# Performance work log

Hardware: AMD Instinct MI355X
Metric: run time of the kernel (lower is better)

## Reference

```python
import jax, jax.numpy as jnp
import numpy as np

H = 8          # heads
D_MODEL = 64   # padded embedding dim (power of 2)
D_K = 8        # per-head dim -> NQ=3 qubits
SEQ = 32
NQ = 3
DIM2 = D_K * D_K  # 2*NQ qubit joint space
W_MUL = float(np.sqrt(2.0) * 5 ** (-0.5))  # PQC he_std * lrmul

# ---- static circuit unitaries (qubit 0 = most significant / leftmost in kron) ----

def _cnot(n, c, t):
    dim = 2 ** n
    P = np.zeros((dim, dim), np.complex64)
    for b in range(dim):
        if (b >> (n - 1 - c)) & 1:
            P[b ^ (1 << (n - 1 - t)), b] = 1.0
        else:
            P[b, b] = 1.0
    return P

def _cnot_ring(n):
    U = np.eye(2 ** n, dtype=np.complex64)
    for t in range(n):
        U = _cnot(n, t, (t + 1) % n) @ U  # later gates multiply on the left
    return U

UC6 = jnp.asarray(_cnot_ring(2 * NQ))  # (64,64) entangling ring used by score + sum circuits
MZ6 = jnp.asarray(((-1.0) ** np.array([bin(i).count('1') for i in range(2 ** (2 * NQ))])).astype(np.complex64))  # Z^{otimes 2n} diagonal

# ---- parameterized single-qubit rotations (batched, differentiable) ----

def _rx(t):
    c = jnp.cos(t / 2).astype(jnp.complex64)
    s = jnp.sin(t / 2).astype(jnp.complex64)
    return jnp.stack([jnp.stack([c, -1j * s], -1), jnp.stack([-1j * s, c], -1)], -2)

def _ry(t):
    c = jnp.cos(t / 2).astype(jnp.complex64)
    s = jnp.sin(t / 2).astype(jnp.complex64)
    return jnp.stack([jnp.stack([c, -s], -1), jnp.stack([s, c], -1)], -2)

def _rz(t):
    e = jnp.exp(-0.5j * t.astype(jnp.complex64))
    z = jnp.zeros_like(e)
    return jnp.stack([jnp.stack([e, z], -1), jnp.stack([z, e.conj()], -1)], -2)

def _kron3(a, b, c):
    out = jnp.einsum('...ad,...be,...cf->...abcdef', a, b, c)
    return out.reshape(out.shape[:-6] + (D_K, D_K))

def _pqc_unitaries(w):
    # w: (H, 3, NQ*3); per qubit apply rx, ry, rz -> per-qubit u = Rz@Ry@Rx, circuit = kron
    a = (w * W_MUL).reshape(H, 3, NQ, 3)
    u = _rz(a[..., 2]) @ _ry(a[..., 1]) @ _rx(a[..., 0])  # (H,3,NQ,2,2)
    return _kron3(u[..., 0, :, :], u[..., 1, :, :], u[..., 2, :, :])  # (H,3,dk,dk)

def _forward(x, pqc_w, W1, b1, W2, b2):
    x = jnp.pad(x, ((0, 0), (0, 0), (0, D_MODEL - x.shape[-1])))
    xq = (x @ W1.T + b1)[0]                                    # (S, d_k) linear1
    psi = xq / jnp.sqrt(jnp.sum(xq * xq, -1, keepdims=True))   # amplitude encoding
    rho = (psi[:, :, None] * psi[:, None, :]).astype(jnp.complex64)  # (S,dk,dk) pure-state density matrices
    Upqc = _pqc_unitaries(pqc_w)                               # (H, 3=[q,k,v], dk, dk)
    rqkv = jnp.einsum('hgab,sbc,hgdc->hgsad', Upqc, rho, Upqc.conj())
    qs, ks_, vs = rqkv[:, 0], rqkv[:, 1], rqkv[:, 2]           # (H,S,dk,dk)
    # score_ij = (Re tr(Z^{2n} U (q_i kron k_j) U^dag) + 1)/2 = (Re tr(A (q kron k)) + 1)/2
    A = (UC6.conj().T * MZ6) @ UC6                             # U^dag Z^{2n} U, (64,64)
    A4 = A.reshape(D_K, D_K, D_K, D_K)                         # [(c,d),(a,b)]
    T = jnp.einsum('cdab,hiac->hidb', A4, qs)
    scores = (jnp.einsum('hidb,hjbd->hij', T, ks_).real + 1.0) * 0.5  # (H,S,S)
    # weighted value: per-qubit rx(phi/2) ry(phi/2) rz(phi) with phi=(score-0.5)*2pi
    phi = (scores - 0.5) * (2.0 * jnp.pi)
    u1 = _rz(phi) @ _ry(phi * 0.5) @ _rx(phi * 0.5)            # (H,S,S,2,2)
    Uw = _kron3(u1, u1, u1)                                    # (H,S,S,dk,dk)
    wvs = Uw @ vs[:, None] @ Uw.conj().swapaxes(-1, -2)        # (H,S_i,S_j,dk,dk)

    def step(rho_a, wv_j):
        # cal_sum fold: kron, entangle with CNOT ring, partial-trace out 2nd register
        rho_ab = jnp.einsum('...ij,...kl->...ikjl', rho_a, wv_j).reshape(H, SEQ, DIM2, DIM2)
        out = UC6 @ rho_ab @ UC6.conj().T
        out = out.reshape(H, SEQ, D_K, D_K, D_K, D_K)
        return jnp.einsum('...abcb->...ac', out), None

    rho_fin, _ = jax.lax.scan(step, wvs[:, :, 0], jnp.moveaxis(wvs[:, :, 1:], 2, 0))
    z = jnp.diagonal(rho_fin, axis1=-2, axis2=-1).real         # (H,S,dk) computational-basis probs
    zs = jnp.transpose(z, (1, 0, 2)).reshape(1, SEQ, H * D_K)  # concat heads
    return zs @ W2.T + b2                                      # linear2; dropout = identity (eval)

def setup_inputs():
    key = jax.random.key(0)
    kk = jax.random.split(key, 4)
    x = jax.random.normal(kk[0], (1, SEQ, D_MODEL), jnp.float32)
    pqc_w = jax.random.uniform(kk[1], (H, 3, NQ * 3), jnp.float32, 0.0, 2.0 * float(np.pi))
    W1 = jax.random.normal(kk[2], (D_K, D_MODEL), jnp.float32) / np.sqrt(D_MODEL).astype(np.float32)
    b1 = jnp.zeros((D_K,), jnp.float32)
    W2 = jax.random.normal(kk[3], (D_MODEL, D_MODEL), jnp.float32) / np.sqrt(D_MODEL).astype(np.float32)
    b2 = jnp.zeros((D_MODEL,), jnp.float32)
    return {"x": x, "pqc_w": pqc_w, "W1": W1, "b1": b1, "W2": W2, "b2": b2, "edge_index": 0}

def reference(x, pqc_w, W1, b1, W2, b2, edge_index):
    # edge_index sentinel 0 == None (dense attention path)
    return _forward(x, pqc_w, W1, b1, W2, b2)
```

## Files before the change

kernel.cpp:

```cpp
#include <hip/hip_runtime.h>
#include <hip/hip_bf16.h>

#define NHEAD 8
#define SEQL  32
#define DKQ   8
static constexpr float W_MUL = 0.632455532033675866f;
static constexpr float PI_F  = 3.14159265358979323846f;

#define WS_Q 0
#define WS_K 256
#define WS_V 512
#define WS_Z 4608

__device__ __forceinline__ float2 cmulf(float2 a, float2 b) {
    return make_float2(a.x*b.x - a.y*b.y, a.x*b.y + a.y*b.x);
}
__device__ __forceinline__ float2 caddf(float2 a, float2 b) {
    return make_float2(a.x + b.x, a.y + b.y);
}
__device__ __forceinline__ int sig3(int a) {
    int a2=(a>>2)&1, a1=(a>>1)&1, a0=a&1;
    return (a2<<2) | ((a1^a2)<<1) | (a0^a1);
}

__global__ __launch_bounds__(256) void k1(const float* __restrict__ x,
                                          const float* __restrict__ pqc_w,
                                          const float* __restrict__ W1,
                                          const float* __restrict__ b1,
                                          float* __restrict__ ws) {
    __shared__ float xq[SEQL][DKQ];
    __shared__ float psi[SEQL][DKQ];
    __shared__ float2 U8[64];

    float* Q  = ws + WS_Q;
    float* K  = ws + WS_K;
    float2* V = (float2*)(ws + WS_V);

    const int t = threadIdx.x;
    const int h = blockIdx.x / 3, g = blockIdx.x % 3;

    {
        const int s = t >> 3, k = t & 7;
        const float4* xr = (const float4*)(x  + s*64);
        const float4* wr = (const float4*)(W1 + k*64);
        float acc = b1[k];
        #pragma unroll
        for (int q = 0; q < 16; ++q) {
            float4 xa = xr[q], wa = wr[q];
            acc += xa.x*wa.x + xa.y*wa.y + xa.z*wa.z + xa.w*wa.w;
        }
        xq[s][k] = acc;
    }
    __syncthreads();
    {
        const int s = t >> 3, k = t & 7;
        float ss = 0.f;
        #pragma unroll
        for (int kk = 0; kk < 8; ++kk) ss += xq[s][kk]*xq[s][kk];
        psi[s][k] = xq[s][k] * rsqrtf(ss);
    }

    if (t < 64) {
        float2 u[3][2][2];
        #pragma unroll
        for (int q = 0; q < 3; ++q) {
            int base = h*27 + g*9 + q*3;
            float t0 = pqc_w[base+0] * W_MUL;
            float t1 = pqc_w[base+1] * W_MUL;
            float t2 = pqc_w[base+2] * W_MUL;
            float c0 = cosf(t0*0.5f), s0 = sinf(t0*0.5f);
            float c1 = cosf(t1*0.5f), s1 = sinf(t1*0.5f);
            float cz = cosf(t2*0.5f), sz = sinf(t2*0.5f);
            float2 m00 = make_float2(c1*c0,  s1*s0);
            float2 m01 = make_float2(-s1*c0, -c1*s0);
            float2 m10 = make_float2(s1*c0,  -c1*s0);
            float2 m11 = make_float2(c1*c0,  -s1*s0);
            float2 em = make_float2(cz, -sz), ep = make_float2(cz, sz);
            u[q][0][0] = cmulf(em, m00);  u[q][0][1] = cmulf(em, m01);
            u[q][1][0] = cmulf(ep, m10);  u[q][1][1] = cmulf(ep, m11);
        }
        int r = t >> 3, c = t & 7;
        U8[t] = cmulf(cmulf(u[0][r>>2][c>>2], u[1][(r>>1)&1][(c>>1)&1]),
                      u[2][r&1][c&1]);
    }
    __syncthreads();

    {
        const int lane = t & 63, wv = t >> 6;
        const int sg = lane >> 3, a = lane & 7;
        const int s = wv*8 + sg;
        float2 phi = make_float2(0.f, 0.f);
        #pragma unroll
        for (int b = 0; b < 8; ++b) {
            float pb = psi[s][b];
            float2 ue = U8[a*8 + b];
            phi.x += ue.x * pb;
            phi.y += ue.y * pb;
        }
        if (g == 2) {
            V[(h*SEQL + s)*8 + a] = phi;
        } else {
            float mag = phi.x*phi.x + phi.y*phi.y;
            float sign = (g == 0) ? ((((a>>2) ^ a) & 1) ? -1.f : 1.f)
                                  : (((a>>1) & 1) ? -1.f : 1.f);
            float val = sign * mag;
            val += __shfl_xor(val, 1, 64);
            val += __shfl_xor(val, 2, 64);
            val += __shfl_xor(val, 4, 64);
            if (a == 0) {
                if (g == 0) Q[h*SEQL + s] = val;
                else        K[h*SEQL + s] = val;
            }
        }
    }
}

__global__ __launch_bounds__(64) void k2(const float* __restrict__ ws,
                                         float* __restrict__ Z) {
    __shared__ __align__(16) float2 Carr[SEQL][4][2];
    __shared__ float2 w0s[8];

    const float*  Q  = ws + WS_Q;
    const float*  Kv = ws + WS_K;
    const float2* V  = (const float2*)(ws + WS_V);

    const int l = threadIdx.x;
    const int h = blockIdx.x >> 5, i = blockIdx.x & 31;
    const float qhi = Q[h*SEQL + i];

    {
        const int j = l & 31, half = l >> 5;
        float phi = PI_F * qhi * Kv[h*SEQL + j];
        float c1 = cosf(phi*0.25f), s1 = sinf(phi*0.25f);
        float ch = cosf(phi*0.5f),  sh = sinf(phi*0.5f);
        float2 em = make_float2(ch, -sh), ep = make_float2(ch, sh);
        float sc = s1*c1;
        float2 u00 = cmulf(em, make_float2(c1*c1,  s1*s1));
        float2 u01 = cmulf(em, make_float2(-sc, -sc));
        float2 u10 = cmulf(ep, make_float2(sc, -sc));
        float2 u11 = cmulf(ep, make_float2(c1*c1, -s1*s1));

        float2 w[8];
        #pragma unroll
        for (int b = 0; b < 8; ++b) w[b] = V[(h*SEQL + j)*8 + b];
        #pragma unroll
        for (int p = 0; p < 4; ++p) {
            float2 lo = w[p], hi = w[p+4];
            w[p]   = caddf(cmulf(u00, lo), cmulf(u01, hi));
            w[p+4] = caddf(cmulf(u10, lo), cmulf(u11, hi));
        }
        #pragma unroll
        for (int p = 0; p < 4; ++p) {
            int i0 = ((p >> 1) << 2) | (p & 1);
            float2 lo = w[i0], hi = w[i0+2];
            w[i0]   = caddf(cmulf(u00, lo), cmulf(u01, hi));
            w[i0+2] = caddf(cmulf(u10, lo), cmulf(u11, hi));
        }
        #pragma unroll
        for (int p = 0; p < 4; ++p) {
            float2 lo = w[2*p], hi = w[2*p+1];
            w[2*p]   = caddf(cmulf(u00, lo), cmulf(u01, hi));
            w[2*p+1] = caddf(cmulf(u10, lo), cmulf(u11, hi));
        }

        if (j == 0 && half == 0) {
            #pragma unroll
            for (int b = 0; b < 8; ++b) w0s[b] = w[b];
        }
        const int mset0[4] = {0,3,5,6}, mset1[4] = {1,2,4,7};
        #pragma unroll
        for (int combo = 0; combo < 4; ++combo) {
            int a0 = combo >> 1, c0 = combo & 1;
            float2 acc = make_float2(0.f, 0.f);
            #pragma unroll
            for (int tt = 0; tt < 4; ++tt) {
                int m = half ? mset1[tt] : mset0[tt];
                float2 wx = w[(a0<<2)^m], wy = w[(c0<<2)^m];
                acc.x += wx.x*wy.x + wx.y*wy.y;
                acc.y += wx.y*wy.x - wx.x*wy.y;
            }
            Carr[j][combo][half] = acc;
        }
    }
    __syncthreads();

    const int a = l >> 3, c = l & 7;
    const int combo = ((a & 1) << 1) | (c & 1);
    const int src0 = (sig3(a) << 3) | sig3(c);
    const int src1 = src0 ^ 54;

    float2 wa = w0s[a], wc = w0s[c];
    float rr = wa.x*wc.x + wa.y*wc.y;
    float ri = wa.y*wc.x - wa.x*wc.y;

    for (int j = 1; j < SEQL; ++j) {
        float4 Cv = *((const float4*)&Carr[j][combo][0]);
        float R0r = __shfl(rr, src0, 64);
        float R0i = __shfl(ri, src0, 64);
        float R1r = __shfl(rr, src1, 64);
        float R1i = __shfl(ri, src1, 64);
        float nr = Cv.x*R0r - Cv.y*R0i + Cv.z*R1r - Cv.w*R1i;
        float ni = Cv.x*R0i + Cv.y*R0r + Cv.z*R1i + Cv.w*R1r;
        rr = nr; ri = ni;
    }
    if (a == c) Z[(h*SEQL + i)*8 + a] = rr;
}

__global__ __launch_bounds__(64) void k3(const float* __restrict__ ws,
                                         const float* __restrict__ W2,
                                         const float* __restrict__ b2,
                                         float* __restrict__ out) {
    const float* Z = ws + WS_Z;
    const int s = blockIdx.x, m = threadIdx.x;
    float acc = b2[m];
    #pragma unroll
    for (int cc = 0; cc < 64; ++cc) {
        float z = Z[(cc >> 3)*256 + s*8 + (cc & 7)];
        acc += z * W2[m*64 + cc];
    }
    out[s*64 + m] = acc;
}

extern "C" void kernel_launch(void* const* d_in, const int* in_sizes, int n_in,
                              void* d_out, int out_size, void* d_ws, size_t ws_size,
                              hipStream_t stream) {
    const float* x     = (const float*)d_in[0];
    const float* pqc_w = (const float*)d_in[1];
    const float* W1    = (const float*)d_in[2];
    const float* b1    = (const float*)d_in[3];
    const float* W2    = (const float*)d_in[4];
    const float* b2    = (const float*)d_in[5];

    float* ws = (float*)d_ws;

    hipLaunchKernelGGL(k1, dim3(24),  dim3(256), 0, stream, x, pqc_w, W1, b1, ws);
    hipLaunchKernelGGL(k2, dim3(256), dim3(64),  0, stream, ws, ws + WS_Z);
    hipLaunchKernelGGL(k3, dim3(32),  dim3(64),  0, stream, ws, W2, b2, (float*)d_out);
}
```

Before: 76.86 us.

## Fuse all three stages into one kernel with redundant per-block recompute

Merges the encoding, score/sum circuit and output-projection kernels into a single launch of 32 blocks with 512 threads, one block per query row and one wave per head. Each block recomputes linear1, normalization, the PQC unitaries and the Q/K/V states in shared memory, so no workspace round trips or extra launches are needed. Linear2 is done from shared Z per row with a shuffle reduction. The cost is heavily redundant recomputation in every block and fewer blocks overall.

```diff
diff --git a/kernel.cpp b/kernel.cpp
--- a/kernel.cpp
+++ b/kernel.cpp
@@ -1,16 +1,9 @@
 #include <hip/hip_runtime.h>
-#include <hip/hip_bf16.h>
 
 #define NHEAD 8
 #define SEQL  32
-#define DKQ   8
 static constexpr float W_MUL = 0.632455532033675866f;
 static constexpr float PI_F  = 3.14159265358979323846f;
-
-#define WS_Q 0
-#define WS_K 256
-#define WS_V 512
-#define WS_Z 4608
 
 __device__ __forceinline__ float2 cmulf(float2 a, float2 b) {
     return make_float2(a.x*b.x - a.y*b.y, a.x*b.y + a.y*b.x);
@@ -23,23 +16,27 @@
     return (a2<<2) | ((a1^a2)<<1) | (a0^a1);
 }
 
-__global__ __launch_bounds__(256) void k1(const float* __restrict__ x,
-                                          const float* __restrict__ pqc_w,
-                                          const float* __restrict__ W1,
-                                          const float* __restrict__ b1,
-                                          float* __restrict__ ws) {
-    __shared__ float xq[SEQL][DKQ];
-    __shared__ float psi[SEQL][DKQ];
-    __shared__ float2 U8[64];
-
-    float* Q  = ws + WS_Q;
-    float* K  = ws + WS_K;
-    float2* V = (float2*)(ws + WS_V);
+__global__ __launch_bounds__(512) void kfused(const float* __restrict__ x,
+                                              const float* __restrict__ pqc_w,
+                                              const float* __restrict__ W1,
+                                              const float* __restrict__ b1,
+                                              const float* __restrict__ W2,
+                                              const float* __restrict__ b2,
+                                              float* __restrict__ out) {
+    __shared__ float  xq[SEQL][8];
+    __shared__ float  psi[SEQL][8];
+    __shared__ float2 us[NHEAD][9][4];
+    __shared__ float2 U8s[NHEAD][3][64];
+    __shared__ __align__(16) float2 Carr[NHEAD][SEQL][4][2];
+    __shared__ float2 w0s[NHEAD][8];
+    __shared__ float  Zs[NHEAD][8];
 
     const int t = threadIdx.x;
-    const int h = blockIdx.x / 3, g = blockIdx.x % 3;
-
-    {
+    const int l = t & 63;
+    const int h = t >> 6;
+    const int i = blockIdx.x;
+
+    if (t < 256) {
         const int s = t >> 3, k = t & 7;
         const float4* xr = (const float4*)(x  + s*64);
         const float4* wr = (const float4*)(W1 + k*64);
@@ -51,88 +48,100 @@
         }
         xq[s][k] = acc;
     }
-    __syncthreads();
-    {
+    if (l < 9) {
+        const int g = l / 3, q = l % 3;
+        const int base = h*27 + g*9 + q*3;
+        float t0 = pqc_w[base+0] * W_MUL;
+        float t1 = pqc_w[base+1] * W_MUL;
+        float t2 = pqc_w[base+2] * W_MUL;
+        float c0, s0, c1, s1, cz, sz;
+        sincosf(t0*0.5f, &s0, &c0);
+        sincosf(t1*0.5f, &s1, &c1);
+        sincosf(t2*0.5f, &sz, &cz);
+        float2 m00 = make_float2(c1*c0,  s1*s0);
+        float2 m01 = make_float2(-s1*c0, -c1*s0);
+        float2 m10 = make_float2(s1*c0,  -c1*s0);
+        float2 m11 = make_float2(c1*c0,  -s1*s0);
+        float2 em = make_float2(cz, -sz), ep = make_float2(cz, sz);
+        us[h][l][0] = cmulf(em, m00);
+        us[h][l][1] = cmulf(em, m01);
+        us[h][l][2] = cmulf(ep, m10);
+        us[h][l][3] = cmulf(ep, m11);
+    }
+    __syncthreads();
+
+    if (t < 256) {
         const int s = t >> 3, k = t & 7;
         float ss = 0.f;
         #pragma unroll
         for (int kk = 0; kk < 8; ++kk) ss += xq[s][kk]*xq[s][kk];
         psi[s][k] = xq[s][k] * rsqrtf(ss);
     }
-
-    if (t < 64) {
-        float2 u[3][2][2];
-        #pragma unroll
-        for (int q = 0; q < 3; ++q) {
-            int base = h*27 + g*9 + q*3;
-            float t0 = pqc_w[base+0] * W_MUL;
-            float t1 = pqc_w[base+1] * W_MUL;
-            float t2 = pqc_w[base+2] * W_MUL;
-            float c0 = cosf(t0*0.5f), s0 = sinf(t0*0.5f);
-            float c1 = cosf(t1*0.5f), s1 = sinf(t1*0.5f);
-            float cz = cosf(t2*0.5f), sz = sinf(t2*0.5f);
-            float2 m00 = make_float2(c1*c0,  s1*s0);
-            float2 m01 = make_float2(-s1*c0, -c1*s0);
-            float2 m10 = make_float2(s1*c0,  -c1*s0);
-            float2 m11 = make_float2(c1*c0,  -s1*s0);
-            float2 em = make_float2(cz, -sz), ep = make_float2(cz, sz);
-            u[q][0][0] = cmulf(em, m00);  u[q][0][1] = cmulf(em, m01);
-            u[q][1][0] = cmulf(ep, m10);  u[q][1][1] = cmulf(ep, m11);
-        }
-        int r = t >> 3, c = t & 7;
-        U8[t] = cmulf(cmulf(u[0][r>>2][c>>2], u[1][(r>>1)&1][(c>>1)&1]),
-                      u[2][r&1][c&1]);
-    }
-    __syncthreads();
-
-    {
-        const int lane = t & 63, wv = t >> 6;
-        const int sg = lane >> 3, a = lane & 7;
-        const int s = wv*8 + sg;
-        float2 phi = make_float2(0.f, 0.f);
-        #pragma unroll
-        for (int b = 0; b < 8; ++b) {
-            float pb = psi[s][b];
-            float2 ue = U8[a*8 + b];
-            phi.x += ue.x * pb;
-            phi.y += ue.y * pb;
-        }
-        if (g == 2) {
-            V[(h*SEQL + s)*8 + a] = phi;
-        } else {
-            float mag = phi.x*phi.x + phi.y*phi.y;
-            float sign = (g == 0) ? ((((a>>2) ^ a) & 1) ? -1.f : 1.f)
-                                  : (((a>>1) & 1) ? -1.f : 1.f);
-            float val = sign * mag;
-            val += __shfl_xor(val, 1, 64);
-            val += __shfl_xor(val, 2, 64);
-            val += __shfl_xor(val, 4, 64);
-            if (a == 0) {
-                if (g == 0) Q[h*SEQL + s] = val;
-                else        K[h*SEQL + s] = val;
-            }
-        }
-    }
-}
-
-__global__ __launch_bounds__(64) void k2(const float* __restrict__ ws,
-                                         float* __restrict__ Z) {
-    __shared__ __align__(16) float2 Carr[SEQL][4][2];
-    __shared__ float2 w0s[8];
-
-    const float*  Q  = ws + WS_Q;
-    const float*  Kv = ws + WS_K;
-    const float2* V  = (const float2*)(ws + WS_V);
-
-    const int l = threadIdx.x;
-    const int h = blockIdx.x >> 5, i = blockIdx.x & 31;
-    const float qhi = Q[h*SEQL + i];
-
-    {
-        const int j = l & 31, half = l >> 5;
-        float phi = PI_F * qhi * Kv[h*SEQL + j];
-        float c1 = cosf(phi*0.25f), s1 = sinf(phi*0.25f);
-        float ch = cosf(phi*0.5f),  sh = sinf(phi*0.5f);
+    {
+        const int r = l >> 3, c = l & 7;
+        const int i0 = ((r>>2)<<1)       | (c>>2);
+        const int i1 = (((r>>1)&1)<<1)   | ((c>>1)&1);
+        const int i2 = ((r&1)<<1)        | (c&1);
+        #pragma unroll
+        for (int g = 0; g < 3; ++g)
+            U8s[h][g][l] = cmulf(cmulf(us[h][g*3+0][i0], us[h][g*3+1][i1]),
+                                 us[h][g*3+2][i2]);
+    }
+    __syncthreads();
+
+    {
+        const int j = l >> 1, half = l & 1;
+
+        float qhi = 0.f;
+        #pragma unroll
+        for (int a = 0; a < 8; ++a) {
+            float2 ph = make_float2(0.f, 0.f);
+            #pragma unroll
+            for (int b = 0; b < 8; ++b) {
+                float pb = psi[i][b];
+                float2 ue = U8s[h][0][a*8 + b];
+                ph.x += ue.x * pb;
+                ph.y += ue.y * pb;
+            }
+            float sign = (((a>>2) ^ a) & 1) ? -1.f : 1.f;
+            qhi += sign * (ph.x*ph.x + ph.y*ph.y);
+        }
+        float kj;
+        {
+            float acc = 0.f;
+            #pragma unroll
+            for (int aa = 0; aa < 4; ++aa) {
+                int a = half*4 + aa;
+                float2 ph = make_float2(0.f, 0.f);
+                #pragma unroll
+                for (int b = 0; b < 8; ++b) {
+                    float pb = psi[j][b];
+                    float2 ue = U8s[h][1][a*8 + b];
+                    ph.x += ue.x * pb;
+                    ph.y += ue.y * pb;
+                }
+                float sign = ((a>>1) & 1) ? -1.f : 1.f;
+                acc += sign * (ph.x*ph.x + ph.y*ph.y);
+            }
+            kj = acc + __shfl_xor(acc, 1, 64);
+        }
+        float2 w[8];
+        #pragma unroll
+        for (int a = 0; a < 8; ++a) {
+            float2 ph = make_float2(0.f, 0.f);
+            #pragma unroll
+            for (int b = 0; b < 8; ++b) {
+                float pb = psi[j][b];
+                float2 ue = U8s[h][2][a*8 + b];
+                ph.x += ue.x * pb;
+                ph.y += ue.y * pb;
+            }
+            w[a] = ph;
+        }
+        float phi = PI_F * qhi * kj;
+        float c1, s1, ch, sh;
+        sincosf(phi*0.25f, &s1, &c1);
+        sincosf(phi*0.5f,  &sh, &ch);
         float2 em = make_float2(ch, -sh), ep = make_float2(ch, sh);
         float sc = s1*c1;
         float2 u00 = cmulf(em, make_float2(c1*c1,  s1*s1));
@@ -140,9 +149,6 @@
         float2 u10 = cmulf(ep, make_float2(sc, -sc));
         float2 u11 = cmulf(ep, make_float2(c1*c1, -s1*s1));
 
-        float2 w[8];
-        #pragma unroll
-        for (int b = 0; b < 8; ++b) w[b] = V[(h*SEQL + j)*8 + b];
         #pragma unroll
         for (int p = 0; p < 4; ++p) {
             float2 lo = w[p], hi = w[p+4];
@@ -163,9 +169,9 @@
             w[2*p+1] = caddf(cmulf(u10, lo), cmulf(u11, hi));
         }
 
-        if (j == 0 && half == 0) {
-            #pragma unroll
-            for (int b = 0; b < 8; ++b) w0s[b] = w[b];
+        if (l == 0) {
+            #pragma unroll
+            for (int b = 0; b < 8; ++b) w0s[h][b] = w[b];
         }
         const int mset0[4] = {0,3,5,6}, mset1[4] = {1,2,4,7};
         #pragma unroll
@@ -179,46 +185,46 @@
                 acc.x += wx.x*wy.x + wx.y*wy.y;
                 acc.y += wx.y*wy.x - wx.x*wy.y;
             }
-            Carr[j][combo][half] = acc;
-        }
-    }
-    __syncthreads();
-
-    const int a = l >> 3, c = l & 7;
-    const int combo = ((a & 1) << 1) | (c & 1);
-    const int src0 = (sig3(a) << 3) | sig3(c);
-    const int src1 = src0 ^ 54;
-
-    float2 wa = w0s[a], wc = w0s[c];
-    float rr = wa.x*wc.x + wa.y*wc.y;
-    float ri = wa.y*wc.x - wa.x*wc.y;
-
-    for (int j = 1; j < SEQL; ++j) {
-        float4 Cv = *((const float4*)&Carr[j][combo][0]);
-        float R0r = __shfl(rr, src0, 64);
-        float R0i = __shfl(ri, src0, 64);
-        float R1r = __shfl(rr, src1, 64);
-        float R1i = __shfl(ri, src1, 64);
-        float nr = Cv.x*R0r - Cv.y*R0i + Cv.z*R1r - Cv.w*R1i;
-        float ni = Cv.x*R0i + Cv.y*R0r + Cv.z*R1i + Cv.w*R1r;
-        rr = nr; ri = ni;
-    }
-    if (a == c) Z[(h*SEQL + i)*8 + a] = rr;
-}
-
-__global__ __launch_bounds__(64) void k3(const float* __restrict__ ws,
-                                         const float* __restrict__ W2,
-                                         const float* __restrict__ b2,
-                                         float* __restrict__ out) {
-    const float* Z = ws + WS_Z;
-    const int s = blockIdx.x, m = threadIdx.x;
-    float acc = b2[m];
-    #pragma unroll
-    for (int cc = 0; cc < 64; ++cc) {
-        float z = Z[(cc >> 3)*256 + s*8 + (cc & 7)];
-        acc += z * W2[m*64 + cc];
-    }
-    out[s*64 + m] = acc;
+            Carr[h][j][combo][half] = acc;
+        }
+    }
+    __syncthreads();
+
+    {
+        const int a = l >> 3, c = l & 7;
+        const int combo = ((a & 1) << 1) | (c & 1);
+        const int src0 = (sig3(a) << 3) | sig3(c);
+        const int src1 = src0 ^ 54;
+
+        float2 wa = w0s[h][a], wc = w0s[h][c];
+        float rr = wa.x*wc.x + wa.y*wc.y;
+        float ri = wa.y*wc.x - wa.x*wc.y;
+
+        for (int j = 1; j < SEQL; ++j) {
+            float4 Cv = *((const float4*)&Carr[h][j][combo][0]);
+            float R0r = __shfl(rr, src0, 64);
+            float R0i = __shfl(ri, src0, 64);
+            float R1r = __shfl(rr, src1, 64);
+            float R1i = __shfl(ri, src1, 64);
+            float nr = Cv.x*R0r - Cv.y*R0i + Cv.z*R1r - Cv.w*R1i;
+            float ni = Cv.x*R0i + Cv.y*R0r + Cv.z*R1i + Cv.w*R1r;
+            rr = nr; ri = ni;
+        }
+        if (a == c) Zs[h][a] = rr;
+    }
+    __syncthreads();
+
+    {
+        const int m = t >> 3, p = t & 7;
+        float acc = 0.f;
+        #pragma unroll
+        for (int cc = 0; cc < 8; ++cc)
+            acc += Zs[p][cc] * W2[m*64 + p*8 + cc];
+        acc += __shfl_xor(acc, 1, 64);
+        acc += __shfl_xor(acc, 2, 64);
+        acc += __shfl_xor(acc, 4, 64);
+        if (p == 0) out[i*64 + m] = acc + b2[m];
+    }
 }
 
 extern "C" void kernel_launch(void* const* d_in, const int* in_sizes, int n_in,
@@ -231,9 +237,6 @@
     const float* W2    = (const float*)d_in[4];
     const float* b2    = (const float*)d_in[5];
 
-    float* ws = (float*)d_ws;
-
-    hipLaunchKernelGGL(k1, dim3(24),  dim3(256), 0, stream, x, pqc_w, W1, b1, ws);
-    hipLaunchKernelGGL(k2, dim3(256), dim3(64),  0, stream, ws, ws + WS_Z);
-    hipLaunchKernelGGL(k3, dim3(32),  dim3(64),  0, stream, ws, W2, b2, (float*)d_out);
-}
+    hipLaunchKernelGGL(kfused, dim3(SEQL), dim3(512), 0, stream,
+                       x, pqc_w, W1, b1, W2, b2, (float*)d_out);
+}
```

After: 81.28 us. +5.7%, slower.
